# Kernel tuning notes

Hardware: AMD Instinct MI355X
Metric: run time of the kernel (lower is better)

The kernel has to match this reference:

```python
import jax, jax.numpy as jnp
import numpy as np

B, L, C = 256, 196, 2048   # batch, conv_att_size, conv_feat_size
E, H, A = 512, 512, 512    # input_encoding_size, lstm_size, att_hidden_size
INITRANGE = 0.1


def _uniform(key, shape):
    return jax.random.uniform(key, shape, jnp.float32, -INITRANGE, INITRANGE)


def setup_inputs() -> dict:
    key = jax.random.key(0)
    ks = jax.random.split(key, 16)
    return {
        "xt": jax.random.normal(ks[0], (B, E), jnp.float32),
        "att_seq": jax.random.normal(ks[1], (B, L, C), jnp.float32),
        "h0": jax.random.normal(ks[2], (1, B, H), jnp.float32),
        "c0": jax.random.normal(ks[3], (1, B, H), jnp.float32),
        # LSTM input projections
        "Wi": _uniform(ks[4], (4 * H, E)), "bi": _uniform(ks[5], (4 * H,)),
        "Wh": _uniform(ks[6], (4 * H, H)), "bh": _uniform(ks[7], (4 * H,)),
        "Wz": _uniform(ks[8], (4 * H, C)), "bz": _uniform(ks[9], (4 * H,)),
        # attention MLP
        "Wa": _uniform(ks[10], (A, C)), "ba": _uniform(ks[11], (A,)),
        "Wha": _uniform(ks[12], (A, H)), "bha": _uniform(ks[13], (A,)),
        "Wo": _uniform(ks[14], (1, A)), "bo": _uniform(ks[15], (1,)),
    }


def reference(xt, att_seq, h0, c0, Wi, bi, Wh, bh, Wz, bz, Wa, ba, Wha, bha, Wo, bo):
    pre_h = h0[-1]  # [B, H]
    pre_c = c0[-1]  # [B, H]

    # attention scoring MLP
    att_linear = jnp.einsum('blc,ac->bla', att_seq, Wa) + ba      # [B, L, A]
    h_linear = pre_h @ Wha.T + bha                                 # [B, A]
    att_h = jnp.tanh(att_linear + h_linear[:, None, :])            # [B, L, A]
    scores = jnp.einsum('bla,a->bl', att_h, Wo[0]) + bo[0]         # [B, L]
    conv_weight = jax.nn.softmax(scores, axis=1)                   # [B, L]

    # weighted sum over attention locations -> context z
    z = jnp.einsum('blc,bl->bc', att_seq, conv_weight)             # [B, C]

    # fused LSTM gates
    all_input_sums = (xt @ Wi.T + bi) + (pre_h @ Wh.T + bh) + (z @ Wz.T + bz)  # [B, 4H]
    gates = jax.nn.sigmoid(all_input_sums[:, :3 * H])
    in_gate = gates[:, :H]
    forget_gate = gates[:, H:2 * H]
    out_gate = gates[:, 2 * H:3 * H]
    in_transform = jnp.tanh(all_input_sums[:, 3 * H:])

    next_c = forget_gate * pre_c + in_gate * in_transform
    next_h = out_gate * jnp.tanh(next_c)
    # dropout is identity in eval mode (deterministic baseline)
    return next_h, next_c
```

## Files before the change

### kernel.cpp

```cpp
#include <hip/hip_runtime.h>
#include <stdint.h>

#define B_ 256
#define L_ 196
#define C_ 2048
#define E_ 512
#define H_ 512
#define A_ 512
#define M_ (B_*L_)

typedef __bf16 bf16x8 __attribute__((ext_vector_type(8)));
typedef float  f32x4  __attribute__((ext_vector_type(4)));

__device__ __forceinline__ unsigned short f2bf(float f) {
    union { float f; unsigned int u; } v; v.f = f;
    unsigned int r = 0x7FFFu + ((v.u >> 16) & 1u);
    return (unsigned short)((v.u + r) >> 16);
}

__device__ __forceinline__ unsigned int pk2(float a, float b) {
    return (unsigned int)f2bf(a) | ((unsigned int)f2bf(b) << 16);
}

__device__ __forceinline__ float tanh_fast(float x) {
    float e = __expf(2.f * x);
    return 1.f - 2.f / (e + 1.f);
}

__device__ __forceinline__ void gload_lds16(const void* g, void* s) {
    __builtin_amdgcn_global_load_lds(
        (const __attribute__((address_space(1))) void*)g,
        (__attribute__((address_space(3))) void*)s, 16, 0, 0);
}


__global__ void k_cvt(const float* __restrict__ src, unsigned short* __restrict__ dst, int n4) {
    int i = blockIdx.x * blockDim.x + threadIdx.x;
    if (i < n4) {
        float4 v = ((const float4*)src)[i];
        ushort4 o; o.x = f2bf(v.x); o.y = f2bf(v.y); o.z = f2bf(v.z); o.w = f2bf(v.w);
        ((ushort4*)dst)[i] = o;
    }
}

__global__ void k_build_wcat(const float* __restrict__ Wi, const float* __restrict__ Wh,
                             const float* __restrict__ Wz, const float* __restrict__ bi,
                             const float* __restrict__ bh, const float* __restrict__ bz,
                             unsigned short* __restrict__ wcat, float* __restrict__ bcat) {
    int j = blockIdx.x;
    int t = threadIdx.x;
    for (int g = t; g < 768; g += 256) {
        int k = g * 4;
        const float* src;
        if (k < 512)       src = Wi + j*512 + k;
        else if (k < 1024) src = Wh + j*512 + (k - 512);
        else               src = Wz + j*2048 + (k - 1024);
        float4 v = *(const float4*)src;
        ushort4 o; o.x = f2bf(v.x); o.y = f2bf(v.y); o.z = f2bf(v.z); o.w = f2bf(v.w);
        *(ushort4*)(wcat + (size_t)j*3072 + k) = o;
    }
    if (t == 0) bcat[j] = bi[j] + bh[j] + bz[j];
}

__global__ void k_build_xcat(const float* __restrict__ xt, const float* __restrict__ preh,
                             unsigned short* __restrict__ xcat) {
    int b = blockIdx.x, t = threadIdx.x;
    const float* src = (t < 128) ? (xt + b*512 + t*4) : (preh + b*512 + (t-128)*4);
    int off = (t < 128) ? (t*4) : (512 + (t-128)*4);
    float4 v = *(const float4*)src;
    ushort4 o; o.x = f2bf(v.x); o.y = f2bf(v.y); o.z = f2bf(v.z); o.w = f2bf(v.w);
    *(ushort4*)(xcat + (size_t)b*3072 + off) = o;
}

__global__ void k_hlin(const float* __restrict__ preh, const float* __restrict__ Wha,
                       const float* __restrict__ bha, const float* __restrict__ ba,
                       float* __restrict__ hlin) {
    __shared__ float ph[512];
    int b = blockIdx.x, t = threadIdx.x;
    ph[t] = preh[b*512 + t];
    __syncthreads();
    float acc = bha[t] + ba[t];
    const float4* wrow = (const float4*)(Wha + (size_t)t*512);
    #pragma unroll 8
    for (int k4 = 0; k4 < 128; ++k4) {
        float4 v = wrow[k4];
        float4 p = *(const float4*)&ph[k4*4];
        acc += v.x*p.x + v.y*p.y + v.z*p.z + v.w*p.w;
    }
    hlin[b*512 + t] = acc;
}


__global__ __launch_bounds__(512, 2) void k_scores(
    const float* __restrict__ att,
    const unsigned short* __restrict__ wa,
    const float* __restrict__ hlin,
    const float* __restrict__ wo,
    const float* __restrict__ bo,
    float* __restrict__ scores)
{
    __shared__ unsigned short smem[40960];
    unsigned short* lA = smem;
    unsigned short* lB = smem + 128*64;

    const int tid = threadIdx.x;
    const int w = tid >> 6, l = tid & 63;
    const int l16 = l & 15, lq = l >> 4;
    const int wr = w >> 2, wc = w & 3;
    const int row0 = blockIdx.x * 128;

    const int ar = tid >> 2;
    const int app = (tid & 3) * 2;

    f32x4 acc[4][8];
    #pragma unroll
    for (int m = 0; m < 4; ++m)
        #pragma unroll
        for (int n = 0; n < 8; ++n) acc[m][n] = (f32x4){0.f, 0.f, 0.f, 0.f};

    for (int kt = 0; kt < C_/64; ++kt) {
        const int k0 = kt * 64;
        __syncthreads();

        #pragma unroll
        for (int i = 0; i < 8; ++i) {
            int g = w*64 + l + i*512;
            int br = g >> 3, bp = g & 7;
            int bps = bp ^ (br & 7);
            gload_lds16(wa + (size_t)br*C_ + k0 + bps*8,
                        lB + (size_t)(w*64 + i*512)*8);
        }

        {
            const float* ga = att + (size_t)(row0 + ar)*C_ + k0 + app*8;
            float4 v0 = *(const float4*)(ga);
            float4 v1 = *(const float4*)(ga + 4);
            float4 v2 = *(const float4*)(ga + 8);
            float4 v3 = *(const float4*)(ga + 12);
            uint4 w0 = make_uint4(pk2(v0.x,v0.y), pk2(v0.z,v0.w), pk2(v1.x,v1.y), pk2(v1.z,v1.w));
            uint4 w1 = make_uint4(pk2(v2.x,v2.y), pk2(v2.z,v2.w), pk2(v3.x,v3.y), pk2(v3.z,v3.w));
            int rs = ar & 7;
            *(uint4*)&lA[ar*64 + ((app     ^ rs) * 8)] = w0;
            *(uint4*)&lA[ar*64 + (((app+1) ^ rs) * 8)] = w1;
        }
        __syncthreads();

        #pragma unroll
        for (int kk = 0; kk < 2; ++kk) {
            bf16x8 af[4];
            #pragma unroll
            for (int m = 0; m < 4; ++m) {
                int rrow = wr*64 + m*16 + l16;
                int c = kk*4 + lq;
                af[m] = *(const bf16x8*)&lA[rrow*64 + ((c ^ (rrow & 7)) * 8)];
            }
            #pragma unroll
            for (int n = 0; n < 8; ++n) {
                int brow = wc*128 + n*16 + l16;
                int c = kk*4 + lq;
                bf16x8 bfr = *(const bf16x8*)&lB[brow*64 + ((c ^ (brow & 7)) * 8)];
                #pragma unroll
                for (int m = 0; m < 4; ++m)
                    acc[m][n] = __builtin_amdgcn_mfma_f32_16x16x32_bf16(af[m], bfr, acc[m][n], 0, 0, 0);
            }
        }
    }

    __syncthreads();
    float* red = (float*)smem;

    const int colbase = wc*128 + l16;
    float won[8], hlA[8], hlB[8];
    const int bA = row0 / L_;
    const int bB = (row0 + 127) / L_;
    const int rsplit = (bA + 1) * L_;
    #pragma unroll
    for (int n = 0; n < 8; ++n) {
        won[n] = wo[colbase + n*16];
        hlA[n] = hlin[bA*A_ + colbase + n*16];
        hlB[n] = hlin[bB*A_ + colbase + n*16];
    }

    #pragma unroll
    for (int m = 0; m < 4; ++m) {
        #pragma unroll
        for (int r = 0; r < 4; ++r) {
            int lrow = wr*64 + m*16 + lq*4 + r;
            int grow = row0 + lrow;
            bool useB = grow >= rsplit;
            float s = 0.f;
            #pragma unroll
            for (int n = 0; n < 8; ++n) {
                float v = acc[m][n][r] + (useB ? hlB[n] : hlA[n]);
                s += tanh_fast(v) * won[n];
            }
            s += __shfl_xor(s, 1);
            s += __shfl_xor(s, 2);
            s += __shfl_xor(s, 4);
            s += __shfl_xor(s, 8);
            if (l16 == 0) red[wc*128 + lrow] = s;
        }
    }
    __syncthreads();
    if (tid < 128) {
        scores[row0 + tid] = red[tid] + red[128 + tid] + red[256 + tid] + red[384 + tid] + bo[0];
    }
}

__global__ void k_softmax(const float* __restrict__ scores, float* __restrict__ cw) {
    __shared__ float sm[4], ss[4];
    int b = blockIdx.x, t = threadIdx.x, w = t >> 6, l = t & 63;
    float v = (t < L_) ? scores[b*L_ + t] : -1e30f;
    float m = v;
    #pragma unroll
    for (int o = 1; o < 64; o <<= 1) m = fmaxf(m, __shfl_xor(m, o));
    if (l == 0) sm[w] = m;
    __syncthreads();
    m = fmaxf(fmaxf(sm[0], sm[1]), fmaxf(sm[2], sm[3]));
    float e = (t < L_) ? expf(v - m) : 0.f;
    float s = e;
    #pragma unroll
    for (int o = 1; o < 64; o <<= 1) s += __shfl_xor(s, o);
    if (l == 0) ss[w] = s;
    __syncthreads();
    s = ss[0] + ss[1] + ss[2] + ss[3];
    if (t < L_) cw[b*L_ + t] = e / s;
}

__global__ void k_z(const float* __restrict__ att, const float* __restrict__ cw,
                    unsigned short* __restrict__ xcat) {
    __shared__ float w_s[L_];
    int b = blockIdx.y, half = blockIdx.x, t = threadIdx.x;
    if (t < L_) w_s[t] = cw[b*L_ + t];
    __syncthreads();
    int c = half*1024 + t*4;
    const float* base = att + (size_t)b*L_*C_ + c;
    float ax = 0.f, ay = 0.f, az = 0.f, aw = 0.f;
    #pragma unroll 4
    for (int li = 0; li < L_; ++li) {
        float4 v = *(const float4*)(base + (size_t)li*C_);
        float wt = w_s[li];
        ax += wt*v.x; ay += wt*v.y; az += wt*v.z; aw += wt*v.w;
    }
    ushort4 o; o.x = f2bf(ax); o.y = f2bf(ay); o.z = f2bf(az); o.w = f2bf(aw);
    *(ushort4*)(xcat + (size_t)b*3072 + 1024 + c) = o;
}

#define K2_LDK 40
__global__ __launch_bounds__(256) void k_gemm2(
    const unsigned short* __restrict__ xcat,
    const unsigned short* __restrict__ wcat,
    const float* __restrict__ bcat,
    float* __restrict__ S)
{
    __shared__ unsigned short lA[64 * K2_LDK];
    __shared__ unsigned short lB[128 * K2_LDK];
    const int tid = threadIdx.x;
    const int w = tid >> 6, l = tid & 63;
    const int l16 = l & 15, lq = l >> 4;
    const int row0 = blockIdx.y * 64;
    const int col0 = blockIdx.x * 128;

    f32x4 acc[4][2];
    #pragma unroll
    for (int m = 0; m < 4; ++m)
        #pragma unroll
        for (int n = 0; n < 2; ++n) acc[m][n] = (f32x4){0.f, 0.f, 0.f, 0.f};

    for (int kt = 0; kt < 3072/32; ++kt) {
        const int k0 = kt * 32;
        __syncthreads();
        {
            int r = tid >> 2, c8 = tid & 3;
            *(uint4*)&lA[r*K2_LDK + c8*8] =
                *(const uint4*)(xcat + (size_t)(row0 + r)*3072 + k0 + c8*8);
        }
        #pragma unroll
        for (int i = 0; i < 2; ++i) {
            int g = tid + i*256;
            int r = g >> 2, c8 = g & 3;
            *(uint4*)&lB[r*K2_LDK + c8*8] =
                *(const uint4*)(wcat + (size_t)(col0 + r)*3072 + k0 + c8*8);
        }
        __syncthreads();

        bf16x8 af[4];
        #pragma unroll
        for (int m = 0; m < 4; ++m)
            af[m] = *(const bf16x8*)&lA[(m*16 + l16)*K2_LDK + lq*8];
        #pragma unroll
        for (int n = 0; n < 2; ++n) {
            bf16x8 bfr = *(const bf16x8*)&lB[(w*32 + n*16 + l16)*K2_LDK + lq*8];
            #pragma unroll
            for (int m = 0; m < 4; ++m)
                acc[m][n] = __builtin_amdgcn_mfma_f32_16x16x32_bf16(af[m], bfr, acc[m][n], 0, 0, 0);
        }
    }

    #pragma unroll
    for (int m = 0; m < 4; ++m)
        #pragma unroll
        for (int n = 0; n < 2; ++n)
            #pragma unroll
            for (int r = 0; r < 4; ++r) {
                int grow = row0 + m*16 + lq*4 + r;
                int col = col0 + w*32 + n*16 + l16;
                S[(size_t)grow*2048 + col] = acc[m][n][r] + bcat[col];
            }
}

__global__ void k_lstm(const float* __restrict__ S, const float* __restrict__ prec,
                       float* __restrict__ out) {
    int b = blockIdx.x, h = threadIdx.x;
    float ig = 1.f / (1.f + expf(-S[(size_t)b*2048 + h]));
    float fg = 1.f / (1.f + expf(-S[(size_t)b*2048 + 512 + h]));
    float og = 1.f / (1.f + expf(-S[(size_t)b*2048 + 1024 + h]));
    float gt = tanhf(S[(size_t)b*2048 + 1536 + h]);
    float c = fg * prec[b*512 + h] + ig * gt;
    out[b*512 + h] = og * tanhf(c);
    out[131072 + b*512 + h] = c;
}

extern "C" void kernel_launch(void* const* d_in, const int* in_sizes, int n_in,
                              void* d_out, int out_size, void* d_ws, size_t ws_size,
                              hipStream_t stream) {
    const float* xt  = (const float*)d_in[0];
    const float* att = (const float*)d_in[1];
    const float* h0  = (const float*)d_in[2];
    const float* c0  = (const float*)d_in[3];
    const float* Wi  = (const float*)d_in[4];
    const float* bi  = (const float*)d_in[5];
    const float* Wh  = (const float*)d_in[6];
    const float* bh  = (const float*)d_in[7];
    const float* Wz  = (const float*)d_in[8];
    const float* bz  = (const float*)d_in[9];
    const float* Wa  = (const float*)d_in[10];
    const float* ba  = (const float*)d_in[11];
    const float* Wha = (const float*)d_in[12];
    const float* bha = (const float*)d_in[13];
    const float* Wo  = (const float*)d_in[14];
    const float* bo  = (const float*)d_in[15];
    float* out = (float*)d_out;

    char* ws = (char*)d_ws;
    unsigned short* wa_bf   = (unsigned short*)(ws);
    unsigned short* wcat_bf = (unsigned short*)(ws + 2097152);
    unsigned short* xcat_bf = (unsigned short*)(ws + 14680064);
    float* hlin   = (float*)(ws + 16252928);
    float* scores = (float*)(ws + 16777216);
    float* cw     = (float*)(ws + 16977920);
    float* bcat   = (float*)(ws + 17178624);
    float* S      = (float*)(ws + 17186816);

    k_cvt<<<1024, 256, 0, stream>>>(Wa, wa_bf, 262144);
    k_build_wcat<<<2048, 256, 0, stream>>>(Wi, Wh, Wz, bi, bh, bz, wcat_bf, bcat);
    k_build_xcat<<<256, 256, 0, stream>>>(xt, h0, xcat_bf);
    k_hlin<<<256, 512, 0, stream>>>(h0, Wha, bha, ba, hlin);
    k_scores<<<M_/128, 512, 0, stream>>>(att, wa_bf, hlin, Wo, bo, scores);
    k_softmax<<<256, 256, 0, stream>>>(scores, cw);
    k_z<<<dim3(2, 256), 256, 0, stream>>>(att, cw, xcat_bf);
    k_gemm2<<<dim3(16, 4), 256, 0, stream>>>(xcat_bf, wcat_bf, bcat, S);
    k_lstm<<<256, 512, 0, stream>>>(S, c0, out);
}
```

Before: 396.9 us.

## Split score GEMM over column blocks with partial sums reduced in softmax

The attention-score GEMM tile shrinks from 128x512 per 512-thread block to 128x128 per 256-thread block, giving 1568 blocks with a swizzled block-to-tile mapping. Each block writes a partial score for its column slice, and the softmax kernel sums the four partials and adds the bias. The aim is more parallelism and occupancy with less LDS per block. The cost is that the fp32 activation tile is read and converted four times instead of once, which raises global traffic on the dominant tensor.

```diff
diff --git a/kernel.cpp b/kernel.cpp
--- a/kernel.cpp
+++ b/kernel.cpp
@@ -91,73 +91,75 @@
 }
 
 
-__global__ __launch_bounds__(512, 2) void k_scores(
+__global__ __launch_bounds__(256, 3) void k_scores(
     const float* __restrict__ att,
     const unsigned short* __restrict__ wa,
     const float* __restrict__ hlin,
     const float* __restrict__ wo,
-    const float* __restrict__ bo,
-    float* __restrict__ scores)
+    float* __restrict__ part)
 {
-    __shared__ unsigned short smem[40960];
+    __shared__ unsigned short smem[128*64 * 2];
     unsigned short* lA = smem;
     unsigned short* lB = smem + 128*64;
 
     const int tid = threadIdx.x;
     const int w = tid >> 6, l = tid & 63;
     const int l16 = l & 15, lq = l >> 4;
-    const int wr = w >> 2, wc = w & 3;
-    const int row0 = blockIdx.x * 128;
-
-    const int ar = tid >> 2;
-    const int app = (tid & 3) * 2;
-
-    f32x4 acc[4][8];
+    const int wr = w >> 1, wc = w & 1;
+
+    const int orig = blockIdx.x;
+    const int wgid = (orig & 7) * 196 + (orig >> 3);
+    const int rowblk = wgid >> 2, colblk = wgid & 3;
+    const int row0 = rowblk * 128;
+    const int colB0 = colblk * 128;
+
+    const int ar = tid >> 1;
+    const int ap0 = (tid & 1) * 4;
+    const int ars = ar & 7;
+
+    f32x4 acc[4][4];
     #pragma unroll
     for (int m = 0; m < 4; ++m)
         #pragma unroll
-        for (int n = 0; n < 8; ++n) acc[m][n] = (f32x4){0.f, 0.f, 0.f, 0.f};
+        for (int n = 0; n < 4; ++n) acc[m][n] = (f32x4){0.f, 0.f, 0.f, 0.f};
 
     for (int kt = 0; kt < C_/64; ++kt) {
         const int k0 = kt * 64;
         __syncthreads();
 
         #pragma unroll
-        for (int i = 0; i < 8; ++i) {
-            int g = w*64 + l + i*512;
+        for (int i = 0; i < 4; ++i) {
+            int g = tid + i*256;
             int br = g >> 3, bp = g & 7;
             int bps = bp ^ (br & 7);
-            gload_lds16(wa + (size_t)br*C_ + k0 + bps*8,
-                        lB + (size_t)(w*64 + i*512)*8);
+            gload_lds16(wa + (size_t)(colB0 + br)*C_ + k0 + bps*8,
+                        lB + (size_t)g*8);
         }
 
         {
-            const float* ga = att + (size_t)(row0 + ar)*C_ + k0 + app*8;
-            float4 v0 = *(const float4*)(ga);
-            float4 v1 = *(const float4*)(ga + 4);
-            float4 v2 = *(const float4*)(ga + 8);
-            float4 v3 = *(const float4*)(ga + 12);
-            uint4 w0 = make_uint4(pk2(v0.x,v0.y), pk2(v0.z,v0.w), pk2(v1.x,v1.y), pk2(v1.z,v1.w));
-            uint4 w1 = make_uint4(pk2(v2.x,v2.y), pk2(v2.z,v2.w), pk2(v3.x,v3.y), pk2(v3.z,v3.w));
-            int rs = ar & 7;
-            *(uint4*)&lA[ar*64 + ((app     ^ rs) * 8)] = w0;
-            *(uint4*)&lA[ar*64 + (((app+1) ^ rs) * 8)] = w1;
+            const float* ga = att + (size_t)(row0 + ar)*C_ + k0 + ap0*8;
+            #pragma unroll
+            for (int j = 0; j < 4; ++j) {
+                float4 a = *(const float4*)(ga + j*8);
+                float4 b = *(const float4*)(ga + j*8 + 4);
+                uint4 wv = make_uint4(pk2(a.x,a.y), pk2(a.z,a.w), pk2(b.x,b.y), pk2(b.z,b.w));
+                *(uint4*)&lA[ar*64 + (((ap0 + j) ^ ars) * 8)] = wv;
+            }
         }
         __syncthreads();
 
         #pragma unroll
         for (int kk = 0; kk < 2; ++kk) {
+            const int c = kk*4 + lq;
             bf16x8 af[4];
             #pragma unroll
             for (int m = 0; m < 4; ++m) {
                 int rrow = wr*64 + m*16 + l16;
-                int c = kk*4 + lq;
                 af[m] = *(const bf16x8*)&lA[rrow*64 + ((c ^ (rrow & 7)) * 8)];
             }
             #pragma unroll
-            for (int n = 0; n < 8; ++n) {
-                int brow = wc*128 + n*16 + l16;
-                int c = kk*4 + lq;
+            for (int n = 0; n < 4; ++n) {
+                int brow = wc*64 + n*16 + l16;
                 bf16x8 bfr = *(const bf16x8*)&lB[brow*64 + ((c ^ (brow & 7)) * 8)];
                 #pragma unroll
                 for (int m = 0; m < 4; ++m)
@@ -169,13 +171,13 @@
     __syncthreads();
     float* red = (float*)smem;
 
-    const int colbase = wc*128 + l16;
-    float won[8], hlA[8], hlB[8];
+    const int colbase = colB0 + wc*64 + l16;
+    float won[4], hlA[4], hlB[4];
     const int bA = row0 / L_;
     const int bB = (row0 + 127) / L_;
     const int rsplit = (bA + 1) * L_;
     #pragma unroll
-    for (int n = 0; n < 8; ++n) {
+    for (int n = 0; n < 4; ++n) {
         won[n] = wo[colbase + n*16];
         hlA[n] = hlin[bA*A_ + colbase + n*16];
         hlB[n] = hlin[bB*A_ + colbase + n*16];
@@ -190,7 +192,7 @@
             bool useB = grow >= rsplit;
             float s = 0.f;
             #pragma unroll
-            for (int n = 0; n < 8; ++n) {
+            for (int n = 0; n < 4; ++n) {
                 float v = acc[m][n][r] + (useB ? hlB[n] : hlA[n]);
                 s += tanh_fast(v) * won[n];
             }
@@ -202,15 +204,19 @@
         }
     }
     __syncthreads();
-    if (tid < 128) {
-        scores[row0 + tid] = red[tid] + red[128 + tid] + red[256 + tid] + red[384 + tid] + bo[0];
-    }
-}
-
-__global__ void k_softmax(const float* __restrict__ scores, float* __restrict__ cw) {
+    if (tid < 128)
+        part[(size_t)colblk*M_ + row0 + tid] = red[tid] + red[128 + tid];
+}
+
+__global__ void k_softmax(const float* __restrict__ part, const float* __restrict__ bo,
+                          float* __restrict__ cw) {
     __shared__ float sm[4], ss[4];
     int b = blockIdx.x, t = threadIdx.x, w = t >> 6, l = t & 63;
-    float v = (t < L_) ? scores[b*L_ + t] : -1e30f;
+    float v = -1e30f;
+    if (t < L_) {
+        int idx = b*L_ + t;
+        v = part[idx] + part[M_ + idx] + part[2*M_ + idx] + part[3*M_ + idx] + bo[0];
+    }
     float m = v;
     #pragma unroll
     for (int o = 1; o < 64; o <<= 1) m = fmaxf(m, __shfl_xor(m, o));
@@ -347,17 +353,17 @@
     unsigned short* wcat_bf = (unsigned short*)(ws + 2097152);
     unsigned short* xcat_bf = (unsigned short*)(ws + 14680064);
     float* hlin   = (float*)(ws + 16252928);
-    float* scores = (float*)(ws + 16777216);
-    float* cw     = (float*)(ws + 16977920);
-    float* bcat   = (float*)(ws + 17178624);
-    float* S      = (float*)(ws + 17186816);
+    float* part   = (float*)(ws + 16777216);
+    float* cw     = (float*)(ws + 17825792);
+    float* bcat   = (float*)(ws + 18087936);
+    float* S      = (float*)(ws + 18096128);
 
     k_cvt<<<1024, 256, 0, stream>>>(Wa, wa_bf, 262144);
     k_build_wcat<<<2048, 256, 0, stream>>>(Wi, Wh, Wz, bi, bh, bz, wcat_bf, bcat);
     k_build_xcat<<<256, 256, 0, stream>>>(xt, h0, xcat_bf);
     k_hlin<<<256, 512, 0, stream>>>(h0, Wha, bha, ba, hlin);
-    k_scores<<<M_/128, 512, 0, stream>>>(att, wa_bf, hlin, Wo, bo, scores);
-    k_softmax<<<256, 256, 0, stream>>>(scores, cw);
+    k_scores<<<1568, 256, 0, stream>>>(att, wa_bf, hlin, Wo, part);
+    k_softmax<<<256, 256, 0, stream>>>(part, bo, cw);
     k_z<<<dim3(2, 256), 256, 0, stream>>>(att, cw, xcat_bf);
     k_gemm2<<<dim3(16, 4), 256, 0, stream>>>(xcat_bf, wcat_bf, bcat, S);
     k_lstm<<<256, 512, 0, stream>>>(S, c0, out);
```

New measurement: 673.7 us. +69.8%, slower.

## Double-buffer LDS tiles in attention score GEMM to overlap loads with MFMA

Applied to the files above, without the earlier changes.

Converts the k_scores main loop to a two-stage software pipeline: the next K-tile of Wa is issued to a second LDS buffer and the next att rows are prefetched into registers while MFMAs run on the current buffer. The bf16 conversion and LDS store for the next tile happen after compute, leaving one barrier per iteration. This doubles LDS to 160KB and drops launch bounds to one block per CU, trading occupancy for overlap of global latency with compute.

```diff
diff --git a/kernel.cpp b/kernel.cpp
--- a/kernel.cpp
+++ b/kernel.cpp
@@ -91,7 +91,7 @@
 }
 
 
-__global__ __launch_bounds__(512, 2) void k_scores(
+__global__ __launch_bounds__(512, 1) void k_scores(
     const float* __restrict__ att,
     const unsigned short* __restrict__ wa,
     const float* __restrict__ hlin,
@@ -99,10 +99,7 @@
     const float* __restrict__ bo,
     float* __restrict__ scores)
 {
-    __shared__ unsigned short smem[40960];
-    unsigned short* lA = smem;
-    unsigned short* lB = smem + 128*64;
-
+    __shared__ unsigned short smem[81920];
     const int tid = threadIdx.x;
     const int w = tid >> 6, l = tid & 63;
     const int l16 = l & 15, lq = l >> 4;
@@ -111,6 +108,9 @@
 
     const int ar = tid >> 2;
     const int app = (tid & 3) * 2;
+    const int ars = ar & 7;
+    const float* gaBase = att + (size_t)(row0 + ar)*C_ + app*8;
+
 
     f32x4 acc[4][8];
     #pragma unroll
@@ -118,55 +118,82 @@
         #pragma unroll
         for (int n = 0; n < 8; ++n) acc[m][n] = (f32x4){0.f, 0.f, 0.f, 0.f};
 
-    for (int kt = 0; kt < C_/64; ++kt) {
-        const int k0 = kt * 64;
-        __syncthreads();
-
+    float4 av[4];
+
+    {
+        const int k0 = 0;
         #pragma unroll
         for (int i = 0; i < 8; ++i) {
-            int g = w*64 + l + i*512;
+            int g = tid + i*512;
             int br = g >> 3, bp = g & 7;
             int bps = bp ^ (br & 7);
             gload_lds16(wa + (size_t)br*C_ + k0 + bps*8,
-                        lB + (size_t)(w*64 + i*512)*8);
-        }
-
-        {
-            const float* ga = att + (size_t)(row0 + ar)*C_ + k0 + app*8;
-            float4 v0 = *(const float4*)(ga);
-            float4 v1 = *(const float4*)(ga + 4);
-            float4 v2 = *(const float4*)(ga + 8);
-            float4 v3 = *(const float4*)(ga + 12);
-            uint4 w0 = make_uint4(pk2(v0.x,v0.y), pk2(v0.z,v0.w), pk2(v1.x,v1.y), pk2(v1.z,v1.w));
-            uint4 w1 = make_uint4(pk2(v2.x,v2.y), pk2(v2.z,v2.w), pk2(v3.x,v3.y), pk2(v3.z,v3.w));
-            int rs = ar & 7;
-            *(uint4*)&lA[ar*64 + ((app     ^ rs) * 8)] = w0;
-            *(uint4*)&lA[ar*64 + (((app+1) ^ rs) * 8)] = w1;
-        }
-        __syncthreads();
+                        smem + 8192 + (size_t)g*8);
+        }
+        const float* ga = gaBase + k0;
+        #pragma unroll
+        for (int j = 0; j < 4; ++j) av[j] = *(const float4*)(ga + j*4);
+        uint4 w0 = make_uint4(pk2(av[0].x,av[0].y), pk2(av[0].z,av[0].w),
+                              pk2(av[1].x,av[1].y), pk2(av[1].z,av[1].w));
+        uint4 w1 = make_uint4(pk2(av[2].x,av[2].y), pk2(av[2].z,av[2].w),
+                              pk2(av[3].x,av[3].y), pk2(av[3].z,av[3].w));
+        *(uint4*)&smem[ar*64 + ((app     ^ ars) * 8)] = w0;
+        *(uint4*)&smem[ar*64 + (((app+1) ^ ars) * 8)] = w1;
+    }
+    __syncthreads();
+
+    for (int kt = 0; kt < 32; ++kt) {
+        unsigned short* lA = smem + (kt & 1) * 40960;
+        unsigned short* lB = lA + 8192;
+        unsigned short* lAn = smem + ((kt & 1) ^ 1) * 40960;
+        unsigned short* lBn = lAn + 8192;
+        const bool has_next = (kt < 31);
+        const int kn = (kt + 1) * 64;
+
+        if (has_next) {
+            #pragma unroll
+            for (int i = 0; i < 8; ++i) {
+                int g = tid + i*512;
+                int br = g >> 3, bp = g & 7;
+                int bps = bp ^ (br & 7);
+                gload_lds16(wa + (size_t)br*C_ + kn + bps*8,
+                            lBn + (size_t)g*8);
+            }
+            const float* ga = gaBase + kn;
+            #pragma unroll
+            for (int j = 0; j < 4; ++j) av[j] = *(const float4*)(ga + j*4);
+        }
 
         #pragma unroll
         for (int kk = 0; kk < 2; ++kk) {
+            const int c = kk*4 + lq;
             bf16x8 af[4];
             #pragma unroll
             for (int m = 0; m < 4; ++m) {
                 int rrow = wr*64 + m*16 + l16;
-                int c = kk*4 + lq;
                 af[m] = *(const bf16x8*)&lA[rrow*64 + ((c ^ (rrow & 7)) * 8)];
             }
             #pragma unroll
             for (int n = 0; n < 8; ++n) {
                 int brow = wc*128 + n*16 + l16;
-                int c = kk*4 + lq;
                 bf16x8 bfr = *(const bf16x8*)&lB[brow*64 + ((c ^ (brow & 7)) * 8)];
                 #pragma unroll
                 for (int m = 0; m < 4; ++m)
                     acc[m][n] = __builtin_amdgcn_mfma_f32_16x16x32_bf16(af[m], bfr, acc[m][n], 0, 0, 0);
             }
         }
-    }
-
-    __syncthreads();
+
+        if (has_next) {
+            uint4 w0 = make_uint4(pk2(av[0].x,av[0].y), pk2(av[0].z,av[0].w),
+                                  pk2(av[1].x,av[1].y), pk2(av[1].z,av[1].w));
+            uint4 w1 = make_uint4(pk2(av[2].x,av[2].y), pk2(av[2].z,av[2].w),
+                                  pk2(av[3].x,av[3].y), pk2(av[3].z,av[3].w));
+            *(uint4*)&lAn[ar*64 + ((app     ^ ars) * 8)] = w0;
+            *(uint4*)&lAn[ar*64 + (((app+1) ^ ars) * 8)] = w1;
+        }
+        __syncthreads();
+    }
+
     float* red = (float*)smem;
 
     const int colbase = wc*128 + l16;
```

After: 355.0 us. 10.5% less time.

## Double-buffer LDS tiles in score GEMM to overlap global loads with MFMA

Applied to the files above, without the earlier changes.

Restructures the k_scores main loop into a software pipeline with two LDS buffers. Weight tiles for the next K step are loaded asynchronously, and activation rows two steps ahead are prefetched into registers, all while MFMAs run on the current tile. Manual vmcnt/lgkmcnt waits and raw barriers replace the two __syncthreads per iteration, and s_setprio raises wave priority around the MFMA blocks. In exchange, occupancy falls to one block per CU (launch bounds 512,1 with doubled shared memory), and correctness depends on the hand-counted wait values.

```diff
diff --git a/kernel.cpp b/kernel.cpp
--- a/kernel.cpp
+++ b/kernel.cpp
@@ -91,7 +91,49 @@
 }
 
 
-__global__ __launch_bounds__(512, 2) void k_scores(
+#define VWAIT8 asm volatile("s_waitcnt vmcnt(8)" ::: "memory")
+#define VWAIT4 asm volatile("s_waitcnt vmcnt(4)" ::: "memory")
+#define VWAIT0 asm volatile("s_waitcnt vmcnt(0)" ::: "memory")
+#define LWAIT0 asm volatile("s_waitcnt lgkmcnt(0)" ::: "memory")
+
+#define ISSUE_B(K0, LBN) do { \
+    _Pragma("unroll") \
+    for (int i_ = 0; i_ < 8; ++i_) \
+        gload_lds16(wa + (size_t)(brow0 + i_*64)*C_ + (K0) + bpsC*8, \
+                    (LBN) + (size_t)(tid + i_*512)*8); \
+} while(0)
+
+#define LOAD_A(K0) do { const float* ga_ = gaBase + (K0); \
+    av0 = *(const float4*)(ga_);      av1 = *(const float4*)(ga_ + 4); \
+    av2 = *(const float4*)(ga_ + 8);  av3 = *(const float4*)(ga_ + 12); \
+} while(0)
+
+#define PACK_A(LAN) do { \
+    uint4 w0_ = make_uint4(pk2(av0.x,av0.y), pk2(av0.z,av0.w), pk2(av1.x,av1.y), pk2(av1.z,av1.w)); \
+    uint4 w1_ = make_uint4(pk2(av2.x,av2.y), pk2(av2.z,av2.w), pk2(av3.x,av3.y), pk2(av3.z,av3.w)); \
+    *(uint4*)&(LAN)[ar*64 + ((app     ^ ars) * 8)] = w0_; \
+    *(uint4*)&(LAN)[ar*64 + (((app+1) ^ ars) * 8)] = w1_; \
+} while(0)
+
+#define COMPUTE(KK, LA, LB) do { \
+    const int c_ = (KK)*4 + lq; \
+    bf16x8 af_[4]; \
+    _Pragma("unroll") \
+    for (int m_ = 0; m_ < 4; ++m_) { \
+        int rrow_ = wr*64 + m_*16 + l16; \
+        af_[m_] = *(const bf16x8*)&(LA)[rrow_*64 + ((c_ ^ (rrow_ & 7)) * 8)]; } \
+    __builtin_amdgcn_s_setprio(1); \
+    _Pragma("unroll") \
+    for (int n_ = 0; n_ < 8; ++n_) { \
+        int brow_ = wc*128 + n_*16 + l16; \
+        bf16x8 bf_ = *(const bf16x8*)&(LB)[brow_*64 + ((c_ ^ (brow_ & 7)) * 8)]; \
+        _Pragma("unroll") \
+        for (int m_ = 0; m_ < 4; ++m_) \
+            acc[m_][n_] = __builtin_amdgcn_mfma_f32_16x16x32_bf16(af_[m_], bf_, acc[m_][n_], 0, 0, 0); } \
+    __builtin_amdgcn_s_setprio(0); \
+} while(0)
+
+__global__ __launch_bounds__(512, 1) void k_scores(
     const float* __restrict__ att,
     const unsigned short* __restrict__ wa,
     const float* __restrict__ hlin,
@@ -99,10 +141,7 @@
     const float* __restrict__ bo,
     float* __restrict__ scores)
 {
-    __shared__ unsigned short smem[40960];
-    unsigned short* lA = smem;
-    unsigned short* lB = smem + 128*64;
-
+    __shared__ unsigned short smem[81920];
     const int tid = threadIdx.x;
     const int w = tid >> 6, l = tid & 63;
     const int l16 = l & 15, lq = l >> 4;
@@ -111,6 +150,11 @@
 
     const int ar = tid >> 2;
     const int app = (tid & 3) * 2;
+    const int ars = ar & 7;
+    const float* gaBase = att + (size_t)(row0 + ar)*C_ + app*8;
+
+    const int brow0 = tid >> 3;
+    const int bpsC = (tid & 7) ^ ((tid >> 3) & 7);
 
     f32x4 acc[4][8];
     #pragma unroll
@@ -118,53 +162,50 @@
         #pragma unroll
         for (int n = 0; n < 8; ++n) acc[m][n] = (f32x4){0.f, 0.f, 0.f, 0.f};
 
-    for (int kt = 0; kt < C_/64; ++kt) {
-        const int k0 = kt * 64;
-        __syncthreads();
-
-        #pragma unroll
-        for (int i = 0; i < 8; ++i) {
-            int g = w*64 + l + i*512;
-            int br = g >> 3, bp = g & 7;
-            int bps = bp ^ (br & 7);
-            gload_lds16(wa + (size_t)br*C_ + k0 + bps*8,
-                        lB + (size_t)(w*64 + i*512)*8);
-        }
-
-        {
-            const float* ga = att + (size_t)(row0 + ar)*C_ + k0 + app*8;
-            float4 v0 = *(const float4*)(ga);
-            float4 v1 = *(const float4*)(ga + 4);
-            float4 v2 = *(const float4*)(ga + 8);
-            float4 v3 = *(const float4*)(ga + 12);
-            uint4 w0 = make_uint4(pk2(v0.x,v0.y), pk2(v0.z,v0.w), pk2(v1.x,v1.y), pk2(v1.z,v1.w));
-            uint4 w1 = make_uint4(pk2(v2.x,v2.y), pk2(v2.z,v2.w), pk2(v3.x,v3.y), pk2(v3.z,v3.w));
-            int rs = ar & 7;
-            *(uint4*)&lA[ar*64 + ((app     ^ rs) * 8)] = w0;
-            *(uint4*)&lA[ar*64 + (((app+1) ^ rs) * 8)] = w1;
-        }
-        __syncthreads();
-
-        #pragma unroll
-        for (int kk = 0; kk < 2; ++kk) {
-            bf16x8 af[4];
-            #pragma unroll
-            for (int m = 0; m < 4; ++m) {
-                int rrow = wr*64 + m*16 + l16;
-                int c = kk*4 + lq;
-                af[m] = *(const bf16x8*)&lA[rrow*64 + ((c ^ (rrow & 7)) * 8)];
-            }
-            #pragma unroll
-            for (int n = 0; n < 8; ++n) {
-                int brow = wc*128 + n*16 + l16;
-                int c = kk*4 + lq;
-                bf16x8 bfr = *(const bf16x8*)&lB[brow*64 + ((c ^ (brow & 7)) * 8)];
-                #pragma unroll
-                for (int m = 0; m < 4; ++m)
-                    acc[m][n] = __builtin_amdgcn_mfma_f32_16x16x32_bf16(af[m], bfr, acc[m][n], 0, 0, 0);
-            }
-        }
-    }
+    float4 av0, av1, av2, av3;
+    unsigned short* lA0 = smem;
+    unsigned short* lB0 = smem + 8192;
+    unsigned short* lA1 = smem + 40960;
+    unsigned short* lB1 = smem + 40960 + 8192;
+
+    LOAD_A(0);
+    ISSUE_B(0, lB0);
+    VWAIT8;
+    PACK_A(lA0);
+    LOAD_A(64);
+    VWAIT4;
+    LWAIT0;
+    __builtin_amdgcn_s_barrier();
+
+    for (int kt = 0; kt < 30; ++kt) {
+        unsigned short* lA  = (kt & 1) ? lA1 : lA0;
+        unsigned short* lB  = (kt & 1) ? lB1 : lB0;
+        unsigned short* lAn = (kt & 1) ? lA0 : lA1;
+        unsigned short* lBn = (kt & 1) ? lB0 : lB1;
+        ISSUE_B((kt + 1) * 64, lBn);
+        COMPUTE(0, lA, lB);
+        VWAIT8;
+        PACK_A(lAn);
+        COMPUTE(1, lA, lB);
+        LOAD_A((kt + 2) * 64);
+        VWAIT4;
+        LWAIT0;
+        __builtin_amdgcn_s_barrier();
+    }
+
+    {
+        ISSUE_B(31 * 64, lB1);
+        COMPUTE(0, lA0, lB0);
+        VWAIT8;
+        PACK_A(lA1);
+        COMPUTE(1, lA0, lB0);
+        VWAIT0;
+        LWAIT0;
+        __builtin_amdgcn_s_barrier();
+    }
+
+    COMPUTE(0, lA1, lB1);
+    COMPUTE(1, lA1, lB1);
 
     __syncthreads();
     float* red = (float*)smem;
```

After: 343.3 us. -13.5%, faster.
